# Performance work log

Measured on AMD Instinct MI355X. Metric: run time of the kernel, lower is better.

The kernel has to match this reference:

```python
import jax, jax.numpy as jnp
import numpy as np

WIN = 9
PAD = WIN // 2
ALPHA = 0.1
BETA = 0.1
EPS_NCC = 1e-5
EPS_SC = 1e-5


def box_sum(x):
    """All-ones WIN^3 box-filter local sum, stride 1, pad WIN//2.
    Implemented separably (3 1-D convs) -- mathematically identical to the
    original single F.conv3d with a ones [1,1,9,9,9] kernel, far cheaper.
    x: [N, 1, D, H, W]"""
    for axis in range(3):
        kshape = [1, 1, 1, 1, 1]
        kshape[2 + axis] = WIN
        kern = jnp.ones(kshape, x.dtype)
        pad = [(0, 0), (0, 0), (0, 0)]
        pad[axis] = (PAD, PAD)
        x = jax.lax.conv_general_dilated(x, kern, (1, 1, 1), pad)
    return x


def setup_inputs() -> dict:
    key = jax.random.key(0)
    k1, k2, k3, k4, k5 = jax.random.split(key, 5)
    B, T, D, H, W = 1, 4, 128, 128, 128
    image = jax.random.normal(k1, (B, T, D, H, W), jnp.float32)
    mask = jax.random.uniform(k2, (B, T, D, H, W), jnp.float32)
    pred_image = jax.random.normal(k3, (B, T, D, H, W), jnp.float32)
    pred_mask = jax.random.uniform(k4, (B, T, D, H, W), jnp.float32)
    flow = jax.random.normal(k5, (T - 1, B, 3, D, H, W), jnp.float32)
    time_diff = jnp.arange(B * T, dtype=jnp.float32).reshape(B, T)
    return {"image": image, "mask": mask, "pred_image": pred_image,
            "pred_mask": pred_mask, "flow": flow, "time_diff": time_diff}


def reference(image, mask, pred_image, pred_mask, flow, time_diff):
    B, T, D, H, W = image.shape
    win_size = WIN ** 3

    # ---- NCC loss: fixed frame (t=0) vs each predicted frame t=1..T-1 ----
    # Per-t (1 - mean(cc_t)) averaged over T-1 equals 1 - mean over the
    # stacked batch since every cc_t has identical shape.
    I = jnp.broadcast_to(image[:, :1], (B, T - 1, D, H, W)).reshape(B * (T - 1), 1, D, H, W)
    J = pred_image[:, 1:].reshape(B * (T - 1), 1, D, H, W)
    I_sum = box_sum(I)
    J_sum = box_sum(J)
    I2_sum = box_sum(I * I)
    J2_sum = box_sum(J * J)
    IJ_sum = box_sum(I * J)
    u_I = I_sum / win_size
    u_J = J_sum / win_size
    cross = IJ_sum - u_J * I_sum - u_I * J_sum + u_I * u_J * win_size
    I_var = I2_sum - 2 * u_I * I_sum + u_I * u_I * win_size
    J_var = J2_sum - 2 * u_J * J_sum + u_J * u_J * win_size
    cc = cross * cross / (I_var * J_var + EPS_NCC)
    ncc = 1.0 - jnp.mean(cc)

    # ---- gradient (flow smoothness) loss, l2 penalty ----
    # flow: [T-1, B, 3, D, H, W]; per-t means of equal-shaped diffs average
    # to the global mean over the leading t axis.
    dy = jnp.square(jnp.abs(flow[:, :, :, 1:, :, :] - flow[:, :, :, :-1, :, :]))
    dx = jnp.square(jnp.abs(flow[:, :, :, :, 1:, :] - flow[:, :, :, :, :-1, :]))
    dz = jnp.square(jnp.abs(flow[:, :, :, :, :, 1:] - flow[:, :, :, :, :, :-1]))
    grad_loss = (jnp.mean(dx) + jnp.mean(dy) + jnp.mean(dz)) / 3.0

    # ---- temporal volume smoothness constraint ----
    area = jnp.sum(pred_mask, axis=(2, 3, 4)).T  # [T, B]
    area = area / jnp.max(area)
    scs = []
    for i in range(T - 2):
        for j in range(i + 1, T - 1):
            for k in range(j + 1, T):
                lam = (time_diff[:, j] - time_diff[:, i] + EPS_SC) / (
                    time_diff[:, k] - time_diff[:, i] + EPS_SC)
                scs.append(jnp.square(area[j] - area[i] - lam * (area[k] - area[i])))
    sc = jnp.mean(jnp.stack(scs, axis=1))

    return ncc + ALPHA * grad_loss + BETA * sc
```

## Files before the change

kernel.cpp:

```cpp
#include <hip/hip_runtime.h>

#define V3 (128 * 128 * 128)

__device__ __forceinline__ float block_reduce(float v, float* sm) {
#pragma unroll
  for (int off = 32; off > 0; off >>= 1) v += __shfl_down(v, off, 64);
  int lane = threadIdx.x & 63;
  int wid  = threadIdx.x >> 6;
  if (lane == 0) sm[wid] = v;
  __syncthreads();
  float r = 0.f;
  if ((int)threadIdx.x < (int)(blockDim.x >> 6)) r = sm[threadIdx.x];
  if (wid == 0) {
#pragma unroll
    for (int off = 4; off > 0; off >>= 1) r += __shfl_down(r, off, 64);
  }
  __syncthreads();
  return r;
}

__device__ __forceinline__ float4 ldz(const float* __restrict__ p, size_t off,
                                      bool v) {
  const float4 q = *(const float4*)(p + off);
  float4 r;
  r.x = v ? q.x : 0.f; r.y = v ? q.y : 0.f;
  r.z = v ? q.z : 0.f; r.w = v ? q.w : 0.f;
  return r;
}

__device__ __forceinline__ void add4(float4& a, const float4 b) {
  a.x += b.x; a.y += b.y; a.z += b.z; a.w += b.w;
}

__device__ __forceinline__ float ccf(float i, float i2, float j, float j2,
                                     float ij) {
  const float inv_win = 1.0f / 729.0f;
  float cross = ij - i * j * inv_win;
  float iv    = i2 - i * i * inv_win;
  float jv    = j2 - j * j * inv_win;
  return cross * cross * __builtin_amdgcn_rcpf(iv * jv + 1e-5f);
}

__global__ __launch_bounds__(256) void area_kernel(const float* __restrict__ pm,
                                                   float* __restrict__ acc) {
  __shared__ float sm[8];
  const int t = blockIdx.y;
  const float* p = pm + (size_t)t * V3;
  const int n4 = V3 / 4;
  float s = 0.f;
  for (int i = blockIdx.x * blockDim.x + threadIdx.x; i < n4;
       i += gridDim.x * blockDim.x) {
    float4 a = *(const float4*)(p + 4 * (size_t)i);
    s += (a.x + a.y) + (a.z + a.w);
  }
  s = block_reduce(s, sm);
  if (threadIdx.x == 0) atomicAdd(acc + t, s);
}

__global__ __launch_bounds__(256) void grad_kernel(const float* __restrict__ fl,
                                                   float* __restrict__ acc) {
  __shared__ float sm[8];
  const int w4 = threadIdx.x & 31;
  const int hl = threadIdx.x >> 5;
  const int h  = blockIdx.x * 8 + hl;
  const int d0 = blockIdx.y * 16;
  const int c  = blockIdx.z;
  const float* p = fl + (size_t)c * V3 + (size_t)h * 128 + w4 * 4;
  const bool hv = (h < 127);

  float s = 0.f;
  float4 cur  = *(const float4*)(p + (size_t)d0 * 16384);
  float4 curh = hv ? *(const float4*)(p + (size_t)d0 * 16384 + 128) : cur;

#pragma unroll
  for (int dd = 0; dd < 16; ++dd) {
    const int d = d0 + dd;
    const bool dv = (d < 127);
    float4 nxt = cur, nxth = curh;
    if (dv) {
      nxt = *(const float4*)(p + (size_t)(d + 1) * 16384);
      if (hv) nxth = *(const float4*)(p + (size_t)(d + 1) * 16384 + 128);
    }
    float x;
    x = cur.y - cur.x; s += x * x;
    x = cur.z - cur.y; s += x * x;
    x = cur.w - cur.z; s += x * x;
    float nx = __shfl_down(cur.x, 1, 64);
    if (w4 != 31) { x = nx - cur.w; s += x * x; }
    if (hv) {
      x = curh.x - cur.x; s += x * x;
      x = curh.y - cur.y; s += x * x;
      x = curh.z - cur.z; s += x * x;
      x = curh.w - cur.w; s += x * x;
    }
    if (dv) {
      x = nxt.x - cur.x; s += x * x;
      x = nxt.y - cur.y; s += x * x;
      x = nxt.z - cur.z; s += x * x;
      x = nxt.w - cur.w; s += x * x;
    }
    cur = nxt; curh = nxth;
  }
  s = block_reduce(s, sm);
  if (threadIdx.x == 0) atomicAdd(acc, s);
}

template <bool WITH_I>
__global__ __launch_bounds__(256) void n1_kernel(const float* __restrict__ I0,
                                                 const float* __restrict__ Jall,
                                                 float* __restrict__ FI,
                                                 float* __restrict__ FJall) {
  constexpr int NF = WITH_I ? 5 : 3;
  __shared__ float sI[2][2][136];
  __shared__ float sJ[2][2][136];
  __shared__ float ring[2][9][NF][128];

  const int tz = blockIdx.z;
  const float* J = Jall + (size_t)tz * V3;
  float* FJ = FJall + (size_t)tz * 3 * (size_t)V3;

  const int w  = threadIdx.x & 127;
  const int dl = threadIdx.x >> 7;
  const int d  = blockIdx.y * 2 + dl;
  const int h0 = blockIdx.x * 16;
  const float* Ib = I0 + (size_t)d * 16384;
  const float* Jb = J  + (size_t)d * 16384;

  if (w < 4) {
    sI[dl][0][w] = 0.f; sI[dl][1][w] = 0.f;
    sJ[dl][0][w] = 0.f; sJ[dl][1][w] = 0.f;
  }
  if (w >= 124) {
    sI[dl][0][w + 8] = 0.f; sI[dl][1][w + 8] = 0.f;
    sJ[dl][0][w + 8] = 0.f; sJ[dl][1][w + 8] = 0.f;
  }
#pragma unroll
  for (int sl = 0; sl < 9; ++sl)
#pragma unroll
    for (int f = 0; f < NF; ++f) ring[dl][sl][f][w] = 0.f;

  auto stage = [&](int hh) {
    if (hh >= 0 && hh < 128) {
      const int b = hh & 1;
      if (w < 32) {
        float4 v = *(const float4*)(Ib + hh * 128 + w * 4);
        *(float4*)&sI[dl][b][4 + w * 4] = v;
      } else if (w < 64) {
        const int l = w - 32;
        float4 v = *(const float4*)(Jb + hh * 128 + l * 4);
        *(float4*)&sJ[dl][b][4 + l * 4] = v;
      }
    }
  };

  float S[NF];
#pragma unroll
  for (int f = 0; f < NF; ++f) S[f] = 0.f;

  stage(h0 - 4);
  int slot = (h0 + 32) % 9;

  for (int hh = h0 - 4; hh < h0 + 20; ++hh) {
    __syncthreads();
    stage(hh + 1);
    const int b = hh & 1;
    const bool valid = (hh >= 0) && (hh < 128);

    float Wn[NF];
#pragma unroll
    for (int f = 0; f < NF; ++f) Wn[f] = 0.f;
    if (valid) {
#pragma unroll
      for (int k = 0; k < 9; ++k) {
        float a = sI[dl][b][w + k];
        float bb = sJ[dl][b][w + k];
        if (WITH_I) {
          Wn[0] += a; Wn[1] += a * a;
          Wn[2] += bb; Wn[3] += bb * bb; Wn[4] += a * bb;
        } else {
          Wn[0] += bb; Wn[1] += bb * bb; Wn[2] += a * bb;
        }
      }
    }

#pragma unroll
    for (int f = 0; f < NF; ++f) {
      float old = ring[dl][slot][f][w];
      ring[dl][slot][f][w] = Wn[f];
      S[f] += Wn[f] - old;
    }
    ++slot; if (slot == 9) slot = 0;

    const int ho = hh - 4;
    if (ho >= h0) {
      size_t base = (size_t)d * 16384 + (size_t)ho * 128 + w;
      if (WITH_I) {
        FI[base]                  = S[0];
        FI[(size_t)V3 + base]     = S[1];
        FJ[base]                  = S[2];
        FJ[(size_t)V3 + base]     = S[3];
        FJ[2 * (size_t)V3 + base] = S[4];
      } else {
        FJ[base]                  = S[0];
        FJ[(size_t)V3 + base]     = S[1];
        FJ[2 * (size_t)V3 + base] = S[2];
      }
    }
  }
}

__global__ __launch_bounds__(256, 2) void n2_kernel(const float* __restrict__ FI,
                                                    const float* __restrict__ FJall,
                                                    float* __restrict__ acc) {
  __shared__ float sm[8];
  const float* FJ = FJall + (size_t)blockIdx.z * 3 * (size_t)V3;
  const int w4 = threadIdx.x & 31;
  const int h  = blockIdx.x * 8 + (threadIdx.x >> 5);
  const int d0 = blockIdx.y * 4;
  const size_t hw = (size_t)h * 128 + w4 * 4;

  const float* P0 = FI;
  const float* P1 = FI + (size_t)V3;
  const float* P2 = FJ;
  const float* P3 = FJ + (size_t)V3;
  const float* P4 = FJ + 2 * (size_t)V3;

  float4 S[4][5];
#pragma unroll
  for (int o = 0; o < 4; ++o)
#pragma unroll
    for (int f = 0; f < 5; ++f) S[o][f] = make_float4(0.f, 0.f, 0.f, 0.f);

#pragma unroll
  for (int k = 0; k < 12; ++k) {
    const int sidx = d0 - 4 + k;
    const bool v = (sidx >= 0) && (sidx < 128);
    const size_t a = (size_t)(v ? sidx : 0) * 16384 + hw;
    float4 q0 = ldz(P0, a, v);
    float4 q1 = ldz(P1, a, v);
    float4 q2 = ldz(P2, a, v);
    float4 q3 = ldz(P3, a, v);
    float4 q4 = ldz(P4, a, v);
#pragma unroll
    for (int o = 0; o < 4; ++o) {
      if (o <= k && k <= o + 8) {
        add4(S[o][0], q0);
        add4(S[o][1], q1);
        add4(S[o][2], q2);
        add4(S[o][3], q3);
        add4(S[o][4], q4);
      }
    }
  }

  float accv = 0.f;
#pragma unroll
  for (int o = 0; o < 4; ++o) {
    accv += ccf(S[o][0].x, S[o][1].x, S[o][2].x, S[o][3].x, S[o][4].x);
    accv += ccf(S[o][0].y, S[o][1].y, S[o][2].y, S[o][3].y, S[o][4].y);
    accv += ccf(S[o][0].z, S[o][1].z, S[o][2].z, S[o][3].z, S[o][4].z);
    accv += ccf(S[o][0].w, S[o][1].w, S[o][2].w, S[o][3].w, S[o][4].w);
  }

  accv = block_reduce(accv, sm);
  if (threadIdx.x == 0) atomicAdd(acc, accv);
}

__global__ void final_kernel(const float* __restrict__ ws,
                             const float* __restrict__ td,
                             float* __restrict__ out) {
  if (threadIdx.x != 0 || blockIdx.x != 0) return;
  float area[4];
  float amax = -1e30f;
#pragma unroll
  for (int t = 0; t < 4; ++t) {
    area[t] = ws[t];
    amax = fmaxf(amax, area[t]);
  }
  float a[4];
#pragma unroll
  for (int t = 0; t < 4; ++t) a[t] = area[t] / amax;

  float sc = 0.f;
  int cnt = 0;
  for (int i = 0; i < 2; ++i)
    for (int j = i + 1; j < 3; ++j)
      for (int k = j + 1; k < 4; ++k) {
        float lam = (td[j] - td[i] + 1e-5f) / (td[k] - td[i] + 1e-5f);
        float e = a[j] - a[i] - lam * (a[k] - a[i]);
        sc += e * e;
        ++cnt;
      }
  sc /= (float)cnt;

  float ncc  = 1.0f - ws[7] / (3.0f * (float)V3);
  float grad = ws[4] / (3.0f * 9.0f * 127.0f * 128.0f * 128.0f);
  out[0] = ncc + 0.1f * grad + 0.1f * sc;
}

extern "C" void kernel_launch(void* const* d_in, const int* in_sizes, int n_in,
                              void* d_out, int out_size, void* d_ws, size_t ws_size,
                              hipStream_t stream) {
  const float* image      = (const float*)d_in[0];
  const float* pred_image = (const float*)d_in[2];
  const float* pred_mask  = (const float*)d_in[3];
  const float* flow       = (const float*)d_in[4];
  const float* time_diff  = (const float*)d_in[5];
  float* out = (float*)d_out;
  float* wsf = (float*)d_ws;
  float* FI  = wsf + 64;
  float* FJ  = FI + 2 * (size_t)V3;

  hipMemsetAsync(d_ws, 0, 256, stream);

  hipLaunchKernelGGL(area_kernel, dim3(512, 4), dim3(256), 0, stream,
                     pred_mask, wsf);
  hipLaunchKernelGGL(grad_kernel, dim3(16, 8, 9), dim3(256), 0, stream,
                     flow, wsf + 4);

  const size_t need_fused = (64 + 11 * (size_t)V3) * sizeof(float);
  if (ws_size >= need_fused) {
    hipLaunchKernelGGL((n1_kernel<true>), dim3(8, 64, 1), dim3(256), 0, stream,
                       image, pred_image + (size_t)V3, FI, FJ);
    hipLaunchKernelGGL((n1_kernel<false>), dim3(8, 64, 2), dim3(256), 0, stream,
                       image, pred_image + 2 * (size_t)V3, FI,
                       FJ + 3 * (size_t)V3);
    hipLaunchKernelGGL(n2_kernel, dim3(16, 32, 3), dim3(256), 0, stream,
                       FI, FJ, wsf + 7);
  } else {
    for (int t = 0; t < 3; ++t) {
      const float* J = pred_image + (size_t)(t + 1) * V3;
      if (t == 0) {
        hipLaunchKernelGGL((n1_kernel<true>), dim3(8, 64, 1), dim3(256), 0,
                           stream, image, J, FI, FJ);
      } else {
        hipLaunchKernelGGL((n1_kernel<false>), dim3(8, 64, 1), dim3(256), 0,
                           stream, image, J, FI, FJ);
      }
      hipLaunchKernelGGL(n2_kernel, dim3(16, 32, 1), dim3(256), 0, stream,
                         FI, FJ, wsf + 7);
    }
  }

  hipLaunchKernelGGL(final_kernel, dim3(1), dim3(1), 0, stream,
                     wsf, time_diff, out);
}
```

Before: 153.9 us.

## Store box-filter intermediates as fp16 and use a sliding-window depth sum in n2

The partial box sums written by n1 are now stored as half precision, which halves the intermediate write and read traffic. The n2 kernel also switches from recomputing a 12-slice window for every 4 outputs to a running sum over 8 output slices, adding one slice and subtracting one per step, with 8-wide vector loads. The risk is accuracy: windowed sums of I^2 and J^2 can reach several hundred, so fp16 rounding, plus drift in the running add/subtract, may disturb the variance cancellation in the NCC term.

```diff
diff --git a/kernel.cpp b/kernel.cpp
--- a/kernel.cpp
+++ b/kernel.cpp
@@ -1,6 +1,9 @@
 #include <hip/hip_runtime.h>
 
 #define V3 (128 * 128 * 128)
+
+typedef _Float16 h8 __attribute__((ext_vector_type(8)));
+typedef float    f8 __attribute__((ext_vector_type(8)));
 
 __device__ __forceinline__ float block_reduce(float v, float* sm) {
 #pragma unroll
@@ -19,26 +22,11 @@
   return r;
 }
 
-__device__ __forceinline__ float4 ldz(const float* __restrict__ p, size_t off,
-                                      bool v) {
-  const float4 q = *(const float4*)(p + off);
-  float4 r;
-  r.x = v ? q.x : 0.f; r.y = v ? q.y : 0.f;
-  r.z = v ? q.z : 0.f; r.w = v ? q.w : 0.f;
-  return r;
-}
-
-__device__ __forceinline__ void add4(float4& a, const float4 b) {
-  a.x += b.x; a.y += b.y; a.z += b.z; a.w += b.w;
-}
-
-__device__ __forceinline__ float ccf(float i, float i2, float j, float j2,
-                                     float ij) {
-  const float inv_win = 1.0f / 729.0f;
-  float cross = ij - i * j * inv_win;
-  float iv    = i2 - i * i * inv_win;
-  float jv    = j2 - j * j * inv_win;
-  return cross * cross * __builtin_amdgcn_rcpf(iv * jv + 1e-5f);
+__device__ __forceinline__ f8 ldh(const _Float16* __restrict__ p, size_t off,
+                                  float m) {
+  h8 q = *(const h8*)(p + off);
+  f8 r = __builtin_convertvector(q, f8);
+  return r * m;
 }
 
 __global__ __launch_bounds__(256) void area_kernel(const float* __restrict__ pm,
@@ -108,8 +96,8 @@
 template <bool WITH_I>
 __global__ __launch_bounds__(256) void n1_kernel(const float* __restrict__ I0,
                                                  const float* __restrict__ Jall,
-                                                 float* __restrict__ FI,
-                                                 float* __restrict__ FJall) {
+                                                 _Float16* __restrict__ FI,
+                                                 _Float16* __restrict__ FJall) {
   constexpr int NF = WITH_I ? 5 : 3;
   __shared__ float sI[2][2][136];
   __shared__ float sJ[2][2][136];
@@ -117,7 +105,7 @@
 
   const int tz = blockIdx.z;
   const float* J = Jall + (size_t)tz * V3;
-  float* FJ = FJall + (size_t)tz * 3 * (size_t)V3;
+  _Float16* FJ = FJall + (size_t)tz * 3 * (size_t)V3;
 
   const int w  = threadIdx.x & 127;
   const int dl = threadIdx.x >> 7;
@@ -195,71 +183,72 @@
     if (ho >= h0) {
       size_t base = (size_t)d * 16384 + (size_t)ho * 128 + w;
       if (WITH_I) {
-        FI[base]                  = S[0];
-        FI[(size_t)V3 + base]     = S[1];
-        FJ[base]                  = S[2];
-        FJ[(size_t)V3 + base]     = S[3];
-        FJ[2 * (size_t)V3 + base] = S[4];
+        FI[base]                  = (_Float16)S[0];
+        FI[(size_t)V3 + base]     = (_Float16)S[1];
+        FJ[base]                  = (_Float16)S[2];
+        FJ[(size_t)V3 + base]     = (_Float16)S[3];
+        FJ[2 * (size_t)V3 + base] = (_Float16)S[4];
       } else {
-        FJ[base]                  = S[0];
-        FJ[(size_t)V3 + base]     = S[1];
-        FJ[2 * (size_t)V3 + base] = S[2];
-      }
-    }
-  }
-}
-
-__global__ __launch_bounds__(256, 2) void n2_kernel(const float* __restrict__ FI,
-                                                    const float* __restrict__ FJall,
-                                                    float* __restrict__ acc) {
+        FJ[base]                  = (_Float16)S[0];
+        FJ[(size_t)V3 + base]     = (_Float16)S[1];
+        FJ[2 * (size_t)V3 + base] = (_Float16)S[2];
+      }
+    }
+  }
+}
+
+__global__ __launch_bounds__(128) void n2_kernel(const _Float16* __restrict__ FI,
+                                                 const _Float16* __restrict__ FJall,
+                                                 float* __restrict__ acc) {
   __shared__ float sm[8];
-  const float* FJ = FJall + (size_t)blockIdx.z * 3 * (size_t)V3;
-  const int w4 = threadIdx.x & 31;
-  const int h  = blockIdx.x * 8 + (threadIdx.x >> 5);
-  const int d0 = blockIdx.y * 4;
-  const size_t hw = (size_t)h * 128 + w4 * 4;
-
-  const float* P0 = FI;
-  const float* P1 = FI + (size_t)V3;
-  const float* P2 = FJ;
-  const float* P3 = FJ + (size_t)V3;
-  const float* P4 = FJ + 2 * (size_t)V3;
-
-  float4 S[4][5];
-#pragma unroll
-  for (int o = 0; o < 4; ++o)
-#pragma unroll
-    for (int f = 0; f < 5; ++f) S[o][f] = make_float4(0.f, 0.f, 0.f, 0.f);
-
-#pragma unroll
-  for (int k = 0; k < 12; ++k) {
-    const int sidx = d0 - 4 + k;
-    const bool v = (sidx >= 0) && (sidx < 128);
-    const size_t a = (size_t)(v ? sidx : 0) * 16384 + hw;
-    float4 q0 = ldz(P0, a, v);
-    float4 q1 = ldz(P1, a, v);
-    float4 q2 = ldz(P2, a, v);
-    float4 q3 = ldz(P3, a, v);
-    float4 q4 = ldz(P4, a, v);
-#pragma unroll
-    for (int o = 0; o < 4; ++o) {
-      if (o <= k && k <= o + 8) {
-        add4(S[o][0], q0);
-        add4(S[o][1], q1);
-        add4(S[o][2], q2);
-        add4(S[o][3], q3);
-        add4(S[o][4], q4);
-      }
-    }
-  }
-
+  const _Float16* FJ = FJall + (size_t)blockIdx.z * 3 * (size_t)V3;
+  const int w8 = threadIdx.x & 15;
+  const int h  = blockIdx.x * 8 + (threadIdx.x >> 4);
+  const int d0 = blockIdx.y * 8;
+  const size_t hw = (size_t)h * 128 + w8 * 8;
+
+  const _Float16* P0 = FI;
+  const _Float16* P1 = FI + (size_t)V3;
+  const _Float16* P2 = FJ;
+  const _Float16* P3 = FJ + (size_t)V3;
+  const _Float16* P4 = FJ + 2 * (size_t)V3;
+
+  f8 S0 = {}, S1 = {}, S2 = {}, S3 = {}, S4 = {};
+#pragma unroll
+  for (int k = 0; k < 9; ++k) {
+    const int dd = d0 - 4 + k;
+    const float m = (dd >= 0) ? 1.f : 0.f;
+    const size_t a = (size_t)(dd >= 0 ? dd : 0) * 16384 + hw;
+    S0 += ldh(P0, a, m);
+    S1 += ldh(P1, a, m);
+    S2 += ldh(P2, a, m);
+    S3 += ldh(P3, a, m);
+    S4 += ldh(P4, a, m);
+  }
+
+  const float inv_win = 1.0f / 729.0f;
   float accv = 0.f;
 #pragma unroll
-  for (int o = 0; o < 4; ++o) {
-    accv += ccf(S[o][0].x, S[o][1].x, S[o][2].x, S[o][3].x, S[o][4].x);
-    accv += ccf(S[o][0].y, S[o][1].y, S[o][2].y, S[o][3].y, S[o][4].y);
-    accv += ccf(S[o][0].z, S[o][1].z, S[o][2].z, S[o][3].z, S[o][4].z);
-    accv += ccf(S[o][0].w, S[o][1].w, S[o][2].w, S[o][3].w, S[o][4].w);
+  for (int dd = 0; dd < 8; ++dd) {
+    const int d = d0 + dd;
+    f8 cross = S4 - S0 * S2 * inv_win;
+    f8 iv    = S1 - S0 * S0 * inv_win;
+    f8 jv    = S3 - S2 * S2 * inv_win;
+    f8 den   = iv * jv + 1e-5f;
+#pragma unroll
+    for (int i = 0; i < 8; ++i)
+      accv += cross[i] * cross[i] * __builtin_amdgcn_rcpf(den[i]);
+
+    const int da = d + 5, ds = d - 4;
+    const float ma = (da < 128) ? 1.f : 0.f;
+    const float ms = (ds >= 0) ? 1.f : 0.f;
+    const size_t aa = (size_t)(da < 128 ? da : 0) * 16384 + hw;
+    const size_t as = (size_t)(ds >= 0 ? ds : 0) * 16384 + hw;
+    S0 += ldh(P0, aa, ma) - ldh(P0, as, ms);
+    S1 += ldh(P1, aa, ma) - ldh(P1, as, ms);
+    S2 += ldh(P2, aa, ma) - ldh(P2, as, ms);
+    S3 += ldh(P3, aa, ma) - ldh(P3, as, ms);
+    S4 += ldh(P4, aa, ma) - ldh(P4, as, ms);
   }
 
   accv = block_reduce(accv, sm);
@@ -308,8 +297,8 @@
   const float* time_diff  = (const float*)d_in[5];
   float* out = (float*)d_out;
   float* wsf = (float*)d_ws;
-  float* FI  = wsf + 64;
-  float* FJ  = FI + 2 * (size_t)V3;
+  _Float16* FI = (_Float16*)(wsf + 64);
+  _Float16* FJ = FI + 2 * (size_t)V3;
 
   hipMemsetAsync(d_ws, 0, 256, stream);
 
@@ -318,14 +307,14 @@
   hipLaunchKernelGGL(grad_kernel, dim3(16, 8, 9), dim3(256), 0, stream,
                      flow, wsf + 4);
 
-  const size_t need_fused = (64 + 11 * (size_t)V3) * sizeof(float);
+  const size_t need_fused = 256 + 11 * (size_t)V3 * sizeof(_Float16);
   if (ws_size >= need_fused) {
     hipLaunchKernelGGL((n1_kernel<true>), dim3(8, 64, 1), dim3(256), 0, stream,
                        image, pred_image + (size_t)V3, FI, FJ);
     hipLaunchKernelGGL((n1_kernel<false>), dim3(8, 64, 2), dim3(256), 0, stream,
                        image, pred_image + 2 * (size_t)V3, FI,
                        FJ + 3 * (size_t)V3);
-    hipLaunchKernelGGL(n2_kernel, dim3(16, 32, 3), dim3(256), 0, stream,
+    hipLaunchKernelGGL(n2_kernel, dim3(16, 16, 3), dim3(128), 0, stream,
                        FI, FJ, wsf + 7);
   } else {
     for (int t = 0; t < 3; ++t) {
@@ -337,7 +326,7 @@
         hipLaunchKernelGGL((n1_kernel<false>), dim3(8, 64, 1), dim3(256), 0,
                            stream, image, J, FI, FJ);
       }
-      hipLaunchKernelGGL(n2_kernel, dim3(16, 32, 1), dim3(256), 0, stream,
+      hipLaunchKernelGGL(n2_kernel, dim3(16, 16, 1), dim3(128), 0, stream,
                          FI, FJ, wsf + 7);
     }
   }
```

Result: faster. 132.5 us (-13.9%).
